# Kernel tuning notes

Hardware: AMD Instinct MI355X
Metric: run time of the kernel (lower is better)

Reference implementation:

```python
import jax, jax.numpy as jnp
import numpy as np

BLOCK_SIZE = 256
HEAD_SIZE = 128
BATCH = 512


def setup_inputs() -> dict:
    key = jax.random.key(0)
    ks = jax.random.split(key, 7)
    s = 1.0 / np.sqrt(HEAD_SIZE)
    x = jax.random.normal(ks[0], (BATCH, BLOCK_SIZE, HEAD_SIZE), dtype=jnp.float32)
    Wk = jax.random.uniform(ks[1], (HEAD_SIZE, HEAD_SIZE), jnp.float32, -s, s)
    bk = jax.random.uniform(ks[2], (HEAD_SIZE,), jnp.float32, -s, s)
    Wq = jax.random.uniform(ks[3], (HEAD_SIZE, HEAD_SIZE), jnp.float32, -s, s)
    bq = jax.random.uniform(ks[4], (HEAD_SIZE,), jnp.float32, -s, s)
    Wv = jax.random.uniform(ks[5], (HEAD_SIZE, HEAD_SIZE), jnp.float32, -s, s)
    bv = jax.random.uniform(ks[6], (HEAD_SIZE,), jnp.float32, -s, s)
    return {"x": x, "Wk": Wk, "bk": bk, "Wq": Wq, "bq": bq, "Wv": Wv, "bv": bv}


def reference(x, Wk, bk, Wq, bq, Wv, bv):
    # Linear layers: y = x @ W.T + b (torch nn.Linear convention)
    k = jnp.einsum('bsd,ed->bse', x, Wk) + bk  # [B,T,H]
    q = jnp.einsum('bsd,ed->bse', x, Wq) + bq
    v = jnp.einsum('bsd,ed->bse', x, Wv) + bv
    # NOTE: original module has NO 1/sqrt(d) scaling — keep faithful.
    scores = jnp.einsum('bqd,bkd->bqk', q, k)  # [B,T,T]
    T = x.shape[1]
    causal = jnp.tril(jnp.ones((T, T), dtype=bool))
    scores = jnp.where(causal, scores, -jnp.inf)
    probs = jax.nn.softmax(scores, axis=-1)
    out = jnp.einsum('bqk,bkd->bqd', probs, v)
    return out
```

## Files before the change

### kernel.cpp

```cpp
#include <hip/hip_runtime.h>
#include <hip/hip_fp16.h>

#define TT 256
#define DD 128
#define NEG -30000.0f

typedef __attribute__((ext_vector_type(4))) float f32x4;
typedef __attribute__((ext_vector_type(8))) _Float16 f16x8;
typedef unsigned int u32;
typedef __attribute__((ext_vector_type(4))) u32 u32x4;
typedef unsigned short u16;

__device__ __forceinline__ u16 tof16(float v) {
  return __builtin_bit_cast(u16, (_Float16)v);
}
__device__ __forceinline__ u32 pkf16(float lo, float hi) {
  return (u32)tof16(lo) | ((u32)tof16(hi) << 16);
}

__device__ __forceinline__ int swz3(int row, int c) {
  return c ^ ((row ^ (row >> 3)) & 7);
}
__device__ __forceinline__ int offR256(int row, int c) {
  return (row << 8) | (swz3(row, c) << 4);
}
__device__ __forceinline__ int offR512(int row, int c) {
  return (row << 9) | (swz3(row, c) << 4);
}
__device__ __forceinline__ int offR256h(int row, int col) {
  return (row << 8) | (swz3(row, col >> 3) << 4) | ((col & 7) << 1);
}
__device__ __forceinline__ int offR512h(int row, int col) {
  return (row << 9) | (swz3(row, col >> 3) << 4) | ((col & 7) << 1);
}

__device__ __forceinline__ f32x4 mfma16(f16x8 a, f16x8 b, f32x4 c) {
  return __builtin_amdgcn_mfma_f32_16x16x32_f16(a, b, c, 0, 0, 0);
}

__global__ void precompute_k(const float* __restrict__ Wk, const float* __restrict__ Wq,
                             const float* __restrict__ bq, const float* __restrict__ Wv,
                             u16* __restrict__ MT, u16* __restrict__ WvB, float* __restrict__ m0) {
  int dp = blockIdx.x;
  int d  = threadIdx.x;
  float acc = 0.f;
  for (int e = 0; e < DD; ++e) acc = fmaf(Wq[e*DD + d], Wk[e*DD + dp], acc);
  MT[dp*DD + d] = tof16(acc);
  WvB[dp*DD + d] = tof16(Wv[dp*DD + d]);
  if (dp == 0) {
    float a0 = 0.f;
    for (int e = 0; e < DD; ++e) a0 = fmaf(bq[e], Wk[e*DD + d], a0);
    m0[d] = a0;
  }
}

template<int MAXT, int MAXC>
__device__ __forceinline__ void attn_sub(int qt, u32x4 (&pf)[MAXC], float& lsum,
                                         const char* bufX, const char* bufA,
                                         int l15, int g) {
  const int nkt = qt + 1;
  const int nch = (nkt + 1) >> 1;
  #pragma unroll
  for (int c = 0; c < MAXC; ++c) { u32x4 z = {0u,0u,0u,0u}; pf[c] = z; }
  f16x8 bA[4];
  #pragma unroll
  for (int kc = 0; kc < 4; ++kc)
    bA[kc] = *(const f16x8*)(bufA + offR256(qt*16 + l15, 4*kc + g));
  f32x4 sacc[MAXT];
  #pragma unroll
  for (int kt = 0; kt < MAXT; ++kt) { f32x4 z = {NEG, NEG, NEG, NEG}; sacc[kt] = z; }
  #pragma unroll
  for (int kt = 0; kt < MAXT; ++kt) {
    if (kt < nkt) {
      f32x4 acc = {0.f, 0.f, 0.f, 0.f};
      #pragma unroll
      for (int kc = 0; kc < 4; ++kc) {
        f16x8 aX = *(const f16x8*)(bufX + offR256(kt*16 + l15, 4*kc + g));
        acc = mfma16(aX, bA[kc], acc);
      }
      if (kt == nkt - 1) {
        #pragma unroll
        for (int j = 0; j < 4; ++j)
          if (g*4 + j > l15) acc[j] = NEG;
      }
      sacc[kt] = acc;
    }
  }
  float mx = NEG;
  #pragma unroll
  for (int kt = 0; kt < MAXT; ++kt) if (kt < nkt) {
    #pragma unroll
    for (int j = 0; j < 4; ++j) mx = fmaxf(mx, sacc[kt][j]);
  }
  mx = fmaxf(mx, __shfl_xor(mx, 16));
  mx = fmaxf(mx, __shfl_xor(mx, 32));
  float sum = 0.f;
  #pragma unroll
  for (int kt = 0; kt < MAXT; ++kt) if (kt < nkt) {
    #pragma unroll
    for (int j = 0; j < 4; ++j) {
      float p = __expf(sacc[kt][j] - mx);
      sacc[kt][j] = p;
      sum += p;
    }
  }
  sum += __shfl_xor(sum, 16);
  sum += __shfl_xor(sum, 32);
  lsum = sum;
  #pragma unroll
  for (int c = 0; c < MAXC; ++c) {
    if (c < nch) {
      u32 p00 = pkf16(sacc[2*c][0], sacc[2*c][1]);
      u32 p01 = pkf16(sacc[2*c][2], sacc[2*c][3]);
      u32 p10 = 0u, p11 = 0u;
      if (2*c + 1 < nkt) {
        p10 = pkf16(sacc[2*c+1][0], sacc[2*c+1][1]);
        p11 = pkf16(sacc[2*c+1][2], sacc[2*c+1][3]);
      }
      u32x4 w;
      #pragma unroll
      for (int wd = 0; wd < 4; ++wd) {
        int src = l15 + 16*((2*g + (wd >> 1)) & 3);
        u32 lo = (u32)__shfl((int)((wd & 1) ? p01 : p00), src, 64);
        u32 hi = (u32)__shfl((int)((wd & 1) ? p11 : p10), src, 64);
        w[wd] = (g >> 1) ? hi : lo;
      }
      pf[c] = w;
    }
  }
}

template<int MAXC>
__device__ __forceinline__ void out_sub(int qt, const u32x4 (&pf)[MAXC], float lsum,
                                        const char* bufVT, const float* __restrict__ bvg,
                                        float* __restrict__ outb, int l15, int g) {
  const int nch = (qt + 2) >> 1;
  const float inv = 1.f / lsum;
  #pragma unroll
  for (int et = 0; et < 8; ++et) {
    f32x4 acc = {0.f, 0.f, 0.f, 0.f};
    #pragma unroll
    for (int c = 0; c < MAXC; ++c) {
      if (c < nch) {
        f16x8 aV = *(const f16x8*)(bufVT + offR512(et*16 + l15, 4*c + g));
        f16x8 pb = __builtin_bit_cast(f16x8, pf[c]);
        acc = mfma16(aV, pb, acc);
      }
    }
    const int q  = qt*16 + l15;
    const int e0 = et*16 + g*4;
    f32x4 bvv = *(const f32x4*)(bvg + e0);
    f32x4 o;
    #pragma unroll
    for (int j = 0; j < 4; ++j) o[j] = acc[j]*inv + bvv[j];
    *(f32x4*)(outb + q*DD + e0) = o;
  }
}

__global__ __launch_bounds__(512, 2)
void head_fused(const float* __restrict__ x, const u16* __restrict__ MTg,
                const u16* __restrict__ Wvg, const float* __restrict__ m0g,
                const float* __restrict__ bvg, float* __restrict__ out) {
  extern __shared__ char lds[];
  char* bufX = lds;
  char* bufA = lds + 65536;
  char* bufW = lds + 131072;

  const int tid  = threadIdx.x;
  const int wave = tid >> 6;
  const int lane = tid & 63;
  const int l15  = lane & 15;
  const int g    = lane >> 4;
  const int b    = blockIdx.x;
  const float* xb = x + (size_t)b * (TT*DD);

  {
    u32x4* p = (u32x4*)lds;
    #pragma unroll
    for (int i = 0; i < 20; ++i) { u32x4 z = {0u,0u,0u,0u}; p[tid + i*512] = z; }
  }
  __syncthreads();

  #pragma unroll
  for (int i = 0; i < 8; ++i) {
    int chunk = tid + i*512;
    int row = chunk >> 4, c = chunk & 15;
    const float* p = xb + row*DD + c*8;
    f32x4 v0 = *(const f32x4*)p;
    f32x4 v1 = *(const f32x4*)(p + 4);
    u32x4 w;
    w[0] = pkf16(v0[0], v0[1]);
    w[1] = pkf16(v0[2], v0[3]);
    w[2] = pkf16(v1[0], v1[1]);
    w[3] = pkf16(v1[2], v1[3]);
    *(u32x4*)(bufX + offR256(row, c)) = w;
  }
  #pragma unroll
  for (int i = 0; i < 4; ++i) {
    int chunk = tid + i*512;
    int row = chunk >> 4, c = chunk & 15;
    u32x4 v = *(const u32x4*)((const char*)MTg + row*256 + c*16);
    *(u32x4*)(bufW + offR256(row, c)) = v;
  }
  __syncthreads();

  #pragma unroll
  for (int s = 0; s < 2; ++s) {
    const int qt = 2*wave + s;
    f16x8 aX[4];
    #pragma unroll
    for (int kc = 0; kc < 4; ++kc)
      aX[kc] = *(const f16x8*)(bufX + offR256(qt*16 + l15, 4*kc + g));
    #pragma unroll
    for (int nt = 0; nt < 8; ++nt) {
      f32x4 acc = {0.f, 0.f, 0.f, 0.f};
      #pragma unroll
      for (int kc = 0; kc < 4; ++kc) {
        f16x8 bM = *(const f16x8*)(bufW + offR256(nt*16 + l15, 4*kc + g));
        acc = mfma16(aX[kc], bM, acc);
      }
      float m0v = m0g[nt*16 + l15];
      #pragma unroll
      for (int j = 0; j < 4; ++j)
        *(u16*)(bufA + offR256h(qt*16 + g*4 + j, nt*16 + l15)) = tof16(acc[j] + m0v);
    }
  }
  __syncthreads();

  u32x4 pf0[4]; u32x4 pf1[8];
  float ls0, ls1;
  attn_sub<8, 4>(wave,       pf0, ls0, bufX, bufA, l15, g);
  attn_sub<16, 8>(15 - wave, pf1, ls1, bufX, bufA, l15, g);
  __syncthreads();

  #pragma unroll
  for (int i = 0; i < 4; ++i) {
    int chunk = tid + i*512;
    int row = chunk >> 4, c = chunk & 15;
    u32x4 v = *(const u32x4*)((const char*)Wvg + row*256 + c*16);
    *(u32x4*)(bufW + offR256(row, c)) = v;
  }
  __syncthreads();

  #pragma unroll
  for (int s = 0; s < 2; ++s) {
    const int kt = 2*wave + s;
    f16x8 bX[4];
    #pragma unroll
    for (int kc = 0; kc < 4; ++kc)
      bX[kc] = *(const f16x8*)(bufX + offR256(kt*16 + l15, 4*kc + g));
    #pragma unroll
    for (int et = 0; et < 8; ++et) {
      f32x4 acc = {0.f, 0.f, 0.f, 0.f};
      #pragma unroll
      for (int kc = 0; kc < 4; ++kc) {
        f16x8 aW = *(const f16x8*)(bufW + offR256(et*16 + l15, 4*kc + g));
        acc = mfma16(aW, bX[kc], acc);
      }
      #pragma unroll
      for (int j = 0; j < 4; ++j)
        *(u16*)(bufA + offR512h(et*16 + g*4 + j, kt*16 + l15)) = tof16(acc[j]);
    }
  }
  __syncthreads();

  float* outb = out + (size_t)b * (TT*DD);
  out_sub<4>(wave,       pf0, ls0, bufA, bvg, outb, l15, g);
  out_sub<8>(15 - wave,  pf1, ls1, bufA, bvg, outb, l15, g);
}

extern "C" void kernel_launch(void* const* d_in, const int* in_sizes, int n_in,
                              void* d_out, int out_size, void* d_ws, size_t ws_size,
                              hipStream_t stream) {
  (void)in_sizes; (void)n_in; (void)out_size; (void)ws_size;
  const float* x  = (const float*)d_in[0];
  const float* Wk = (const float*)d_in[1];
  const float* Wq = (const float*)d_in[3];
  const float* bq = (const float*)d_in[4];
  const float* Wv = (const float*)d_in[5];
  const float* bv = (const float*)d_in[6];

  char* ws = (char*)d_ws;
  u16*   MT  = (u16*)ws;
  u16*   WvB = (u16*)(ws + 32768);
  float* m0  = (float*)(ws + 65536);

  (void)hipFuncSetAttribute((const void*)head_fused,
                            hipFuncAttributeMaxDynamicSharedMemorySize, 163840);

  precompute_k<<<128, 128, 0, stream>>>(Wk, Wq, bq, Wv, MT, WvB, m0);
  head_fused<<<512, 512, 163840, stream>>>(x, MT, WvB, m0, bv, (float*)d_out);
}
```

Before: 100.2 us.

## Use 1024-thread blocks with one query tile per wave, weights read from global

Doubles the block to 16 waves so each wave owns a single query tile, instead of the balanced pair of short and long causal tiles per wave. The LDS weight staging buffer is removed, and the projection matrices are read directly from global memory into MFMA operands, cutting shared memory from 160KB to 128KB. This aims at more waves to hide latency and less LDS traffic. In exchange it brings heavy load imbalance across waves, unswizzled global weight loads, and an aggressive launch bound that may force register spills.

```diff
diff --git a/kernel.cpp b/kernel.cpp
--- a/kernel.cpp
+++ b/kernel.cpp
@@ -54,23 +54,22 @@
   }
 }
 
-template<int MAXT, int MAXC>
-__device__ __forceinline__ void attn_sub(int qt, u32x4 (&pf)[MAXC], float& lsum,
+__device__ __forceinline__ void attn_sub(int qt, u32x4 (&pf)[8], float& lsum,
                                          const char* bufX, const char* bufA,
                                          int l15, int g) {
   const int nkt = qt + 1;
   const int nch = (nkt + 1) >> 1;
   #pragma unroll
-  for (int c = 0; c < MAXC; ++c) { u32x4 z = {0u,0u,0u,0u}; pf[c] = z; }
+  for (int c = 0; c < 8; ++c) { u32x4 z = {0u,0u,0u,0u}; pf[c] = z; }
   f16x8 bA[4];
   #pragma unroll
   for (int kc = 0; kc < 4; ++kc)
     bA[kc] = *(const f16x8*)(bufA + offR256(qt*16 + l15, 4*kc + g));
-  f32x4 sacc[MAXT];
-  #pragma unroll
-  for (int kt = 0; kt < MAXT; ++kt) { f32x4 z = {NEG, NEG, NEG, NEG}; sacc[kt] = z; }
-  #pragma unroll
-  for (int kt = 0; kt < MAXT; ++kt) {
+  f32x4 sacc[16];
+  #pragma unroll
+  for (int kt = 0; kt < 16; ++kt) { f32x4 z = {NEG, NEG, NEG, NEG}; sacc[kt] = z; }
+  #pragma unroll
+  for (int kt = 0; kt < 16; ++kt) {
     if (kt < nkt) {
       f32x4 acc = {0.f, 0.f, 0.f, 0.f};
       #pragma unroll
@@ -88,7 +87,7 @@
   }
   float mx = NEG;
   #pragma unroll
-  for (int kt = 0; kt < MAXT; ++kt) if (kt < nkt) {
+  for (int kt = 0; kt < 16; ++kt) if (kt < nkt) {
     #pragma unroll
     for (int j = 0; j < 4; ++j) mx = fmaxf(mx, sacc[kt][j]);
   }
@@ -96,7 +95,7 @@
   mx = fmaxf(mx, __shfl_xor(mx, 32));
   float sum = 0.f;
   #pragma unroll
-  for (int kt = 0; kt < MAXT; ++kt) if (kt < nkt) {
+  for (int kt = 0; kt < 16; ++kt) if (kt < nkt) {
     #pragma unroll
     for (int j = 0; j < 4; ++j) {
       float p = __expf(sacc[kt][j] - mx);
@@ -108,7 +107,7 @@
   sum += __shfl_xor(sum, 32);
   lsum = sum;
   #pragma unroll
-  for (int c = 0; c < MAXC; ++c) {
+  for (int c = 0; c < 8; ++c) {
     if (c < nch) {
       u32 p00 = pkf16(sacc[2*c][0], sacc[2*c][1]);
       u32 p01 = pkf16(sacc[2*c][2], sacc[2*c][3]);
@@ -130,8 +129,7 @@
   }
 }
 
-template<int MAXC>
-__device__ __forceinline__ void out_sub(int qt, const u32x4 (&pf)[MAXC], float lsum,
+__device__ __forceinline__ void out_sub(int qt, const u32x4 (&pf)[8], float lsum,
                                         const char* bufVT, const float* __restrict__ bvg,
                                         float* __restrict__ outb, int l15, int g) {
   const int nch = (qt + 2) >> 1;
@@ -140,7 +138,7 @@
   for (int et = 0; et < 8; ++et) {
     f32x4 acc = {0.f, 0.f, 0.f, 0.f};
     #pragma unroll
-    for (int c = 0; c < MAXC; ++c) {
+    for (int c = 0; c < 8; ++c) {
       if (c < nch) {
         f16x8 aV = *(const f16x8*)(bufVT + offR512(et*16 + l15, 4*c + g));
         f16x8 pb = __builtin_bit_cast(f16x8, pf[c]);
@@ -157,14 +155,13 @@
   }
 }
 
-__global__ __launch_bounds__(512, 2)
+__global__ __launch_bounds__(1024, 4)
 void head_fused(const float* __restrict__ x, const u16* __restrict__ MTg,
                 const u16* __restrict__ Wvg, const float* __restrict__ m0g,
                 const float* __restrict__ bvg, float* __restrict__ out) {
   extern __shared__ char lds[];
   char* bufX = lds;
   char* bufA = lds + 65536;
-  char* bufW = lds + 131072;
 
   const int tid  = threadIdx.x;
   const int wave = tid >> 6;
@@ -177,13 +174,13 @@
   {
     u32x4* p = (u32x4*)lds;
     #pragma unroll
-    for (int i = 0; i < 20; ++i) { u32x4 z = {0u,0u,0u,0u}; p[tid + i*512] = z; }
-  }
-  __syncthreads();
-
-  #pragma unroll
-  for (int i = 0; i < 8; ++i) {
-    int chunk = tid + i*512;
+    for (int i = 0; i < 8; ++i) { u32x4 z = {0u,0u,0u,0u}; p[tid + i*1024] = z; }
+  }
+  __syncthreads();
+
+  #pragma unroll
+  for (int i = 0; i < 4; ++i) {
+    int chunk = tid + i*1024;
     int row = chunk >> 4, c = chunk & 15;
     const float* p = xb + row*DD + c*8;
     f32x4 v0 = *(const f32x4*)p;
@@ -195,18 +192,10 @@
     w[3] = pkf16(v1[2], v1[3]);
     *(u32x4*)(bufX + offR256(row, c)) = w;
   }
-  #pragma unroll
-  for (int i = 0; i < 4; ++i) {
-    int chunk = tid + i*512;
-    int row = chunk >> 4, c = chunk & 15;
-    u32x4 v = *(const u32x4*)((const char*)MTg + row*256 + c*16);
-    *(u32x4*)(bufW + offR256(row, c)) = v;
-  }
-  __syncthreads();
-
-  #pragma unroll
-  for (int s = 0; s < 2; ++s) {
-    const int qt = 2*wave + s;
+  __syncthreads();
+
+  {
+    const int qt = wave;
     f16x8 aX[4];
     #pragma unroll
     for (int kc = 0; kc < 4; ++kc)
@@ -216,7 +205,7 @@
       f32x4 acc = {0.f, 0.f, 0.f, 0.f};
       #pragma unroll
       for (int kc = 0; kc < 4; ++kc) {
-        f16x8 bM = *(const f16x8*)(bufW + offR256(nt*16 + l15, 4*kc + g));
+        f16x8 bM = *(const f16x8*)(MTg + (nt*16 + l15)*DD + kc*32 + g*8);
         acc = mfma16(aX[kc], bM, acc);
       }
       float m0v = m0g[nt*16 + l15];
@@ -227,24 +216,13 @@
   }
   __syncthreads();
 
-  u32x4 pf0[4]; u32x4 pf1[8];
-  float ls0, ls1;
-  attn_sub<8, 4>(wave,       pf0, ls0, bufX, bufA, l15, g);
-  attn_sub<16, 8>(15 - wave, pf1, ls1, bufX, bufA, l15, g);
-  __syncthreads();
-
-  #pragma unroll
-  for (int i = 0; i < 4; ++i) {
-    int chunk = tid + i*512;
-    int row = chunk >> 4, c = chunk & 15;
-    u32x4 v = *(const u32x4*)((const char*)Wvg + row*256 + c*16);
-    *(u32x4*)(bufW + offR256(row, c)) = v;
-  }
-  __syncthreads();
-
-  #pragma unroll
-  for (int s = 0; s < 2; ++s) {
-    const int kt = 2*wave + s;
+  u32x4 pf[8];
+  float ls;
+  attn_sub(wave, pf, ls, bufX, bufA, l15, g);
+  __syncthreads();
+
+  {
+    const int kt = wave;
     f16x8 bX[4];
     #pragma unroll
     for (int kc = 0; kc < 4; ++kc)
@@ -254,7 +232,7 @@
       f32x4 acc = {0.f, 0.f, 0.f, 0.f};
       #pragma unroll
       for (int kc = 0; kc < 4; ++kc) {
-        f16x8 aW = *(const f16x8*)(bufW + offR256(et*16 + l15, 4*kc + g));
+        f16x8 aW = *(const f16x8*)(Wvg + (et*16 + l15)*DD + kc*32 + g*8);
         acc = mfma16(aW, bX[kc], acc);
       }
       #pragma unroll
@@ -265,8 +243,7 @@
   __syncthreads();
 
   float* outb = out + (size_t)b * (TT*DD);
-  out_sub<4>(wave,       pf0, ls0, bufA, bvg, outb, l15, g);
-  out_sub<8>(15 - wave,  pf1, ls1, bufA, bvg, outb, l15, g);
+  out_sub(wave, pf, ls, bufA, bvg, outb, l15, g);
 }
 
 extern "C" void kernel_launch(void* const* d_in, const int* in_sizes, int n_in,
@@ -286,8 +263,8 @@
   float* m0  = (float*)(ws + 65536);
 
   (void)hipFuncSetAttribute((const void*)head_fused,
-                            hipFuncAttributeMaxDynamicSharedMemorySize, 163840);
+                            hipFuncAttributeMaxDynamicSharedMemorySize, 131072);
 
   precompute_k<<<128, 128, 0, stream>>>(Wk, Wq, bq, Wv, MT, WvB, m0);
-  head_fused<<<512, 512, 163840, stream>>>(x, MT, WvB, m0, bv, (float*)d_out);
-}
+  head_fused<<<512, 1024, 131072, stream>>>(x, MT, WvB, m0, bv, (float*)d_out);
+}
```

New measurement: 113.8 us. 13.5% more time.

## Split fused attention into projection and per-query-tile attention kernels via workspace

Applied to the files above, without the earlier changes.

Replaces the single LDS-heavy fused kernel with two kernels. The first converts x to fp16 and computes V^T into global workspace in an MFMA-fragment-friendly layout. The second launches 2048 blocks, each taking one query tile per wave, with no LDS and an interleaved block-to-batch mapping. The aim is higher occupancy and parallelism than the 160KB-LDS, 512-block design, paid for with extra global traffic for xh and vt and an extra launch. The old fused path is kept as a fallback when the workspace is too small.

```diff
diff --git a/kernel.cpp b/kernel.cpp
--- a/kernel.cpp
+++ b/kernel.cpp
@@ -17,25 +17,28 @@
 __device__ __forceinline__ u32 pkf16(float lo, float hi) {
   return (u32)tof16(lo) | ((u32)tof16(hi) << 16);
 }
-
-__device__ __forceinline__ int swz3(int row, int c) {
-  return c ^ ((row ^ (row >> 3)) & 7);
-}
-__device__ __forceinline__ int offR256(int row, int c) {
-  return (row << 8) | (swz3(row, c) << 4);
-}
-__device__ __forceinline__ int offR512(int row, int c) {
-  return (row << 9) | (swz3(row, c) << 4);
-}
-__device__ __forceinline__ int offR256h(int row, int col) {
-  return (row << 8) | (swz3(row, col >> 3) << 4) | ((col & 7) << 1);
-}
-__device__ __forceinline__ int offR512h(int row, int col) {
-  return (row << 9) | (swz3(row, col >> 3) << 4) | ((col & 7) << 1);
-}
-
 __device__ __forceinline__ f32x4 mfma16(f16x8 a, f16x8 b, f32x4 c) {
   return __builtin_amdgcn_mfma_f32_16x16x32_f16(a, b, c, 0, 0, 0);
+}
+
+template<int P>
+__device__ __forceinline__ void convN(const f32x4* src, u32x4* dst, int l15, int g) {
+  #pragma unroll
+  for (int p = 0; p < P; ++p) {
+    u32 p00 = pkf16(src[2*p][0], src[2*p][1]);
+    u32 p01 = pkf16(src[2*p][2], src[2*p][3]);
+    u32 p10 = pkf16(src[2*p+1][0], src[2*p+1][1]);
+    u32 p11 = pkf16(src[2*p+1][2], src[2*p+1][3]);
+    u32x4 w;
+    #pragma unroll
+    for (int wd = 0; wd < 4; ++wd) {
+      int srcl = l15 + 16*((2*g + (wd >> 1)) & 3);
+      u32 lo = (u32)__shfl((int)((wd & 1) ? p01 : p00), srcl, 64);
+      u32 hi = (u32)__shfl((int)((wd & 1) ? p11 : p10), srcl, 64);
+      w[wd] = (g >> 1) ? hi : lo;
+    }
+    dst[p] = w;
+  }
 }
 
 __global__ void precompute_k(const float* __restrict__ Wk, const float* __restrict__ Wq,
@@ -54,10 +57,197 @@
   }
 }
 
+__global__ __launch_bounds__(256, 4)
+void proj_vt(const float* __restrict__ x, const u16* __restrict__ WvB,
+             char* __restrict__ xh, char* __restrict__ vt) {
+  const int tid = threadIdx.x;
+  const int w = tid >> 6, lane = tid & 63, l15 = lane & 15, g = lane >> 4;
+  const int b = blockIdx.x;
+  const float* xb = x + (size_t)b * (TT*DD);
+  char* xhb = xh + (size_t)b * 65536;
+  char* vtb = vt + (size_t)b * 65536;
+
+  f16x8 bX[4][4];
+  #pragma unroll
+  for (int t = 0; t < 4; ++t) {
+    const int kt = 4*w + t;
+    #pragma unroll
+    for (int kc = 0; kc < 4; ++kc) {
+      const float* p = xb + (kt*16 + l15)*DD + kc*32 + g*8;
+      f32x4 v0 = *(const f32x4*)p, v1 = *(const f32x4*)(p + 4);
+      u32x4 pk;
+      pk[0] = pkf16(v0[0], v0[1]); pk[1] = pkf16(v0[2], v0[3]);
+      pk[2] = pkf16(v1[0], v1[1]); pk[3] = pkf16(v1[2], v1[3]);
+      bX[t][kc] = __builtin_bit_cast(f16x8, pk);
+      *(u32x4*)(xhb + kt*4096 + kc*1024 + g*256 + l15*16) = pk;
+    }
+  }
+
+  #pragma unroll
+  for (int et = 0; et < 8; ++et) {
+    f16x8 bWv[4];
+    #pragma unroll
+    for (int kc = 0; kc < 4; ++kc)
+      bWv[kc] = *(const f16x8*)(WvB + (et*16 + l15)*DD + kc*32 + g*8);
+    f32x4 vacc[4];
+    #pragma unroll
+    for (int t = 0; t < 4; ++t) {
+      f32x4 acc = {0.f, 0.f, 0.f, 0.f};
+      #pragma unroll
+      for (int kc = 0; kc < 4; ++kc) acc = mfma16(bX[t][kc], bWv[kc], acc);
+      vacc[t] = acc;
+    }
+    u32x4 dv[2];
+    convN<2>(vacc, dv, l15, g);
+    #pragma unroll
+    for (int p2 = 0; p2 < 2; ++p2)
+      *(u32x4*)(vtb + et*8192 + (2*w + p2)*1024 + g*256 + l15*16) = dv[p2];
+  }
+}
+
+__global__ __launch_bounds__(256, 4)
+void attn_k(const char* __restrict__ xh, const char* __restrict__ vt,
+            const u16* __restrict__ MTg, const float* __restrict__ m0g,
+            const float* __restrict__ bvg, float* __restrict__ out) {
+  const int tid  = threadIdx.x;
+  const int wave = tid >> 6, lane = tid & 63, l15 = lane & 15, g = lane >> 4;
+  const int bid = blockIdx.x;
+  const int L   = (bid & 7) * 256 + (bid >> 3);
+  const int b   = L >> 2;
+  const int s   = L & 3;
+  const int qt  = wave*4 + s;
+  const int nkt = qt + 1;
+  const int nch = (nkt + 1) >> 1;
+  const char* xhb = xh + (size_t)b * 65536;
+
+  f16x8 bXq[4];
+  #pragma unroll
+  for (int kc = 0; kc < 4; ++kc)
+    bXq[kc] = *(const f16x8*)(xhb + qt*4096 + kc*1024 + g*256 + l15*16);
+  f32x4 Aacc[8];
+  #pragma unroll
+  for (int dt = 0; dt < 8; ++dt) {
+    f32x4 acc = {0.f, 0.f, 0.f, 0.f};
+    #pragma unroll
+    for (int kc = 0; kc < 4; ++kc) {
+      f16x8 aM = *(const f16x8*)(MTg + (dt*16 + l15)*DD + kc*32 + g*8);
+      acc = mfma16(aM, bXq[kc], acc);
+    }
+    f32x4 m0v = *(const f32x4*)(m0g + dt*16 + g*4);
+    #pragma unroll
+    for (int j = 0; j < 4; ++j) acc[j] += m0v[j];
+    Aacc[dt] = acc;
+  }
+  u32x4 bAw[4];
+  convN<4>(Aacc, bAw, l15, g);
+
+  f32x4 sacc[16];
+  #pragma unroll
+  for (int kt = 0; kt < 16; ++kt) { f32x4 z = {NEG, NEG, NEG, NEG}; sacc[kt] = z; }
+  #pragma unroll
+  for (int kt = 0; kt < 16; ++kt) {
+    if (kt < nkt) {
+      f32x4 acc = {0.f, 0.f, 0.f, 0.f};
+      #pragma unroll
+      for (int kc = 0; kc < 4; ++kc) {
+        f16x8 aX = *(const f16x8*)(xhb + kt*4096 + kc*1024 + g*256 + l15*16);
+        acc = mfma16(aX, __builtin_bit_cast(f16x8, bAw[kc]), acc);
+      }
+      if (kt == nkt - 1) {
+        #pragma unroll
+        for (int j = 0; j < 4; ++j)
+          if (g*4 + j > l15) acc[j] = NEG;
+      }
+      sacc[kt] = acc;
+    }
+  }
+  float mx = NEG;
+  #pragma unroll
+  for (int kt = 0; kt < 16; ++kt) if (kt < nkt) {
+    #pragma unroll
+    for (int j = 0; j < 4; ++j) mx = fmaxf(mx, sacc[kt][j]);
+  }
+  mx = fmaxf(mx, __shfl_xor(mx, 16));
+  mx = fmaxf(mx, __shfl_xor(mx, 32));
+  float sum = 0.f;
+  #pragma unroll
+  for (int kt = 0; kt < 16; ++kt) if (kt < nkt) {
+    #pragma unroll
+    for (int j = 0; j < 4; ++j) {
+      float p = __expf(sacc[kt][j] - mx);
+      sacc[kt][j] = p;
+      sum += p;
+    }
+  }
+  sum += __shfl_xor(sum, 16);
+  sum += __shfl_xor(sum, 32);
+  const float inv = 1.f / sum;
+
+  u32x4 pf[8];
+  #pragma unroll
+  for (int c = 0; c < 8; ++c) { u32x4 z = {0u,0u,0u,0u}; pf[c] = z; }
+  #pragma unroll
+  for (int c = 0; c < 8; ++c) {
+    if (c < nch) {
+      u32 p00 = pkf16(sacc[2*c][0], sacc[2*c][1]);
+      u32 p01 = pkf16(sacc[2*c][2], sacc[2*c][3]);
+      u32 p10 = 0u, p11 = 0u;
+      if (2*c + 1 < nkt) {
+        p10 = pkf16(sacc[2*c+1][0], sacc[2*c+1][1]);
+        p11 = pkf16(sacc[2*c+1][2], sacc[2*c+1][3]);
+      }
+      u32x4 w;
+      #pragma unroll
+      for (int wd = 0; wd < 4; ++wd) {
+        int srcl = l15 + 16*((2*g + (wd >> 1)) & 3);
+        u32 lo = (u32)__shfl((int)((wd & 1) ? p01 : p00), srcl, 64);
+        u32 hi = (u32)__shfl((int)((wd & 1) ? p11 : p10), srcl, 64);
+        w[wd] = (g >> 1) ? hi : lo;
+      }
+      pf[c] = w;
+    }
+  }
+
+  const char* vtb = vt + (size_t)b * 65536;
+  float* outb = out + (size_t)b * (TT*DD);
+  #pragma unroll
+  for (int et = 0; et < 8; ++et) {
+    f32x4 oacc = {0.f, 0.f, 0.f, 0.f};
+    #pragma unroll
+    for (int c = 0; c < 8; ++c) {
+      if (c < nch) {
+        f16x8 aV = *(const f16x8*)(vtb + et*8192 + c*1024 + g*256 + l15*16);
+        oacc = mfma16(aV, __builtin_bit_cast(f16x8, pf[c]), oacc);
+      }
+    }
+    f32x4 bvv = *(const f32x4*)(bvg + et*16 + g*4);
+    f32x4 o;
+    #pragma unroll
+    for (int j = 0; j < 4; ++j) o[j] = oacc[j]*inv + bvv[j];
+    *(f32x4*)(outb + (qt*16 + l15)*DD + et*16 + g*4) = o;
+  }
+}
+
+__device__ __forceinline__ int swz3(int row, int c) {
+  return c ^ ((row ^ (row >> 3)) & 7);
+}
+__device__ __forceinline__ int offR256(int row, int c) {
+  return (row << 8) | (swz3(row, c) << 4);
+}
+__device__ __forceinline__ int offR512(int row, int c) {
+  return (row << 9) | (swz3(row, c) << 4);
+}
+__device__ __forceinline__ int offR256h(int row, int col) {
+  return (row << 8) | (swz3(row, col >> 3) << 4) | ((col & 7) << 1);
+}
+__device__ __forceinline__ int offR512h(int row, int col) {
+  return (row << 9) | (swz3(row, col >> 3) << 4) | ((col & 7) << 1);
+}
+
 template<int MAXT, int MAXC>
-__device__ __forceinline__ void attn_sub(int qt, u32x4 (&pf)[MAXC], float& lsum,
-                                         const char* bufX, const char* bufA,
-                                         int l15, int g) {
+__device__ __forceinline__ void attn_sub_fb(int qt, u32x4 (&pf)[MAXC], float& lsum,
+                                            const char* bufX, const char* bufA,
+                                            int l15, int g) {
   const int nkt = qt + 1;
   const int nch = (nkt + 1) >> 1;
   #pragma unroll
@@ -131,9 +321,9 @@
 }
 
 template<int MAXC>
-__device__ __forceinline__ void out_sub(int qt, const u32x4 (&pf)[MAXC], float lsum,
-                                        const char* bufVT, const float* __restrict__ bvg,
-                                        float* __restrict__ outb, int l15, int g) {
+__device__ __forceinline__ void out_sub_fb(int qt, const u32x4 (&pf)[MAXC], float lsum,
+                                           const char* bufVT, const float* __restrict__ bvg,
+                                           float* __restrict__ outb, int l15, int g) {
   const int nch = (qt + 2) >> 1;
   const float inv = 1.f / lsum;
   #pragma unroll
@@ -158,9 +348,9 @@
 }
 
 __global__ __launch_bounds__(512, 2)
-void head_fused(const float* __restrict__ x, const u16* __restrict__ MTg,
-                const u16* __restrict__ Wvg, const float* __restrict__ m0g,
-                const float* __restrict__ bvg, float* __restrict__ out) {
+void head_fused_fb(const float* __restrict__ x, const u16* __restrict__ MTg,
+                   const u16* __restrict__ Wvg, const float* __restrict__ m0g,
+                   const float* __restrict__ bvg, float* __restrict__ out) {
   extern __shared__ char lds[];
   char* bufX = lds;
   char* bufA = lds + 65536;
@@ -229,8 +419,8 @@
 
   u32x4 pf0[4]; u32x4 pf1[8];
   float ls0, ls1;
-  attn_sub<8, 4>(wave,       pf0, ls0, bufX, bufA, l15, g);
-  attn_sub<16, 8>(15 - wave, pf1, ls1, bufX, bufA, l15, g);
+  attn_sub_fb<8, 4>(wave,       pf0, ls0, bufX, bufA, l15, g);
+  attn_sub_fb<16, 8>(15 - wave, pf1, ls1, bufX, bufA, l15, g);
   __syncthreads();
 
   #pragma unroll
@@ -265,14 +455,14 @@
   __syncthreads();
 
   float* outb = out + (size_t)b * (TT*DD);
-  out_sub<4>(wave,       pf0, ls0, bufA, bvg, outb, l15, g);
-  out_sub<8>(15 - wave,  pf1, ls1, bufA, bvg, outb, l15, g);
+  out_sub_fb<4>(wave,       pf0, ls0, bufA, bvg, outb, l15, g);
+  out_sub_fb<8>(15 - wave,  pf1, ls1, bufA, bvg, outb, l15, g);
 }
 
 extern "C" void kernel_launch(void* const* d_in, const int* in_sizes, int n_in,
                               void* d_out, int out_size, void* d_ws, size_t ws_size,
                               hipStream_t stream) {
-  (void)in_sizes; (void)n_in; (void)out_size; (void)ws_size;
+  (void)in_sizes; (void)n_in; (void)out_size;
   const float* x  = (const float*)d_in[0];
   const float* Wk = (const float*)d_in[1];
   const float* Wq = (const float*)d_in[3];
@@ -281,13 +471,28 @@
   const float* bv = (const float*)d_in[6];
 
   char* ws = (char*)d_ws;
-  u16*   MT  = (u16*)ws;
-  u16*   WvB = (u16*)(ws + 32768);
-  float* m0  = (float*)(ws + 65536);
-
-  (void)hipFuncSetAttribute((const void*)head_fused,
-                            hipFuncAttributeMaxDynamicSharedMemorySize, 163840);
-
-  precompute_k<<<128, 128, 0, stream>>>(Wk, Wq, bq, Wv, MT, WvB, m0);
-  head_fused<<<512, 512, 163840, stream>>>(x, MT, WvB, m0, bv, (float*)d_out);
-}
+  const size_t XH_BYTES = (size_t)512 * 65536;
+  const size_t VT_BYTES = (size_t)512 * 65536;
+  const size_t need = XH_BYTES + VT_BYTES + 65536 + 512;
+
+  if (ws_size >= need) {
+    char*  xhp = ws;
+    char*  vtp = ws + XH_BYTES;
+    char*  wts = ws + XH_BYTES + VT_BYTES;
+    u16*   MT  = (u16*)wts;
+    u16*   WvB = (u16*)(wts + 32768);
+    float* m0  = (float*)(wts + 65536);
+
+    precompute_k<<<128, 128, 0, stream>>>(Wk, Wq, bq, Wv, MT, WvB, m0);
+    proj_vt<<<512, 256, 0, stream>>>(x, WvB, xhp, vtp);
+    attn_k<<<2048, 256, 0, stream>>>(xhp, vtp, MT, m0, bv, (float*)d_out);
+  } else {
+    u16*   MT  = (u16*)ws;
+    u16*   WvB = (u16*)(ws + 32768);
+    float* m0  = (float*)(ws + 65536);
+    (void)hipFuncSetAttribute((const void*)head_fused_fb,
+                              hipFuncAttributeMaxDynamicSharedMemorySize, 163840);
+    precompute_k<<<128, 128, 0, stream>>>(Wk, Wq, bq, Wv, MT, WvB, m0);
+    head_fused_fb<<<512, 512, 163840, stream>>>(x, MT, WvB, m0, bv, (float*)d_out);
+  }
+}
```

Result: slower. 117.1 us (+16.9%).
